# Optimization experiments

Measured on AMD Instinct MI355X. Metric: run time of the kernel, lower is better.

## Reference

```python
import jax, jax.numpy as jnp
import numpy as np

# Synthetic layered DAG: 8 node-layers of width N -> 7 masked dense layers.
B = 4096        # batch
N = 2048        # nodes per DAG layer (= in_features = out_features)
DEPTH = 7       # number of weight layers (len(L) - 1)
DENSITY = 0.25  # fraction of predecessor edges present (mask sparsity)


def setup_inputs() -> dict:
    key = jax.random.key(0)
    kx, kw, km = jax.random.split(key, 3)
    x = jax.random.normal(kx, (B, N), dtype=jnp.float32)
    # Mask M: [DEPTH, N+1, N]; random 0/1 edges, last row (bias) all ones.
    m = (jax.random.uniform(km, (DEPTH, N + 1, N)) < DENSITY).astype(jnp.float32)
    M = m.at[:, -1, :].set(1.0)
    # Kaiming-uniform per column: bound = 1/sqrt(nnz_j) (torch code's init),
    # nonzero only at masked positions (W initialized to zeros elsewhere).
    nnz = jnp.maximum(M.sum(axis=1, keepdims=True), 1.0)  # [DEPTH,1,N]
    u = jax.random.uniform(kw, (DEPTH, N + 1, N), minval=-1.0, maxval=1.0)
    W = (u / jnp.sqrt(nnz)) * M
    return {"x": x, "W": W, "M": M}


def reference(x, W, M):
    # activations buffer semantics collapse to a per-layer chain because each
    # layer's preds are exactly the previous DAG layer; sinks = last layer.
    def step(acts, wm):
        w, m = wm  # [N+1, N] each
        h = jnp.concatenate(
            [acts, jnp.ones((acts.shape[0], 1), acts.dtype)], axis=1)  # [B, N+1]
        acts = jax.nn.relu(h @ (m * w))  # masked dense matmul + ReLU
        return acts, None

    out, _ = jax.lax.scan(step, x, (W, M))
    return out  # [B, N] activations of sink nodes
```

## Files before the change

kernel.cpp:

```cpp
#include <hip/hip_runtime.h>
#include <hip/hip_bf16.h>

typedef __bf16 bf16_t;
typedef __bf16 v8bf __attribute__((ext_vector_type(8)));
typedef __bf16 v4bf __attribute__((ext_vector_type(4)));
typedef float  v4f  __attribute__((ext_vector_type(4)));

#define B_ROWS 4096
#define N_COLS 2048
#define K_FULL 2049
#define KK     2048
#define DEPTH  7

#define BM 128
#define BN 128
#define BK 128
#define NKT (KK / BK)

__global__ __launch_bounds__(256) void wt_kernel(const float* __restrict__ W,
                                                 bf16_t* __restrict__ Wt,
                                                 float* __restrict__ Bias) {
  __shared__ float t[64][129];
  const int l  = blockIdx.z;
  const int k0 = blockIdx.x * 128;
  const int n0 = blockIdx.y * 64;
  const int tid = threadIdx.x;
  const int r   = tid >> 4;
  const int c4  = (tid & 15) * 4;
  const float* Wl = W + (size_t)l * K_FULL * N_COLS;
#pragma unroll
  for (int it = 0; it < 8; ++it) {
    const int kk = r + it * 16;
    const float4 v = *(const float4*)&Wl[(size_t)(k0 + kk) * N_COLS + n0 + c4];
    t[c4 + 0][kk] = v.x;
    t[c4 + 1][kk] = v.y;
    t[c4 + 2][kk] = v.z;
    t[c4 + 3][kk] = v.w;
  }
  if (k0 == 0 && tid < 16) {
    *(float4*)&Bias[(size_t)l * N_COLS + n0 + tid * 4] =
        *(const float4*)&Wl[(size_t)KK * N_COLS + n0 + tid * 4];
  }
  __syncthreads();
  bf16_t* Wtl = Wt + (size_t)l * N_COLS * KK;
  const int g = tid & 15;
#pragma unroll
  for (int it = 0; it < 4; ++it) {
    const int n = r + it * 16;
    v8bf o;
#pragma unroll
    for (int j = 0; j < 8; ++j) o[j] = (bf16_t)t[n][g * 8 + j];
    *(v8bf*)&Wtl[(size_t)(n0 + n) * KK + k0 + g * 8] = o;
  }
}

__global__ __launch_bounds__(256) void init_kernel(const float* __restrict__ x,
                                                   bf16_t* __restrict__ A0) {
  const int c4 = (blockIdx.x * 256 + threadIdx.x) * 4;
  const int r  = blockIdx.y;
  const float4 v = *(const float4*)&x[(size_t)r * N_COLS + c4];
  v4bf o;
  o[0] = (bf16_t)v.x; o[1] = (bf16_t)v.y; o[2] = (bf16_t)v.z; o[3] = (bf16_t)v.w;
  *(v4bf*)&A0[(size_t)r * N_COLS + c4] = o;
}

__global__ __launch_bounds__(512, 4) void gemm_kernel(
    const bf16_t* __restrict__ A, const bf16_t* __restrict__ Bt,
    const float* __restrict__ bias,
    bf16_t* __restrict__ Cn, float* __restrict__ Co) {
  __shared__ __align__(16) char smem[65536];
  bf16_t* As = (bf16_t*)smem;
  bf16_t* Bs = (bf16_t*)(smem + 32768);

  const int bid = blockIdx.x;
  const int swz = (bid & 7) * 64 + (bid >> 3);
  const int bx  = swz & 15;
  const int by  = swz >> 4;

  const int tid  = threadIdx.x;
  const int wave = tid >> 6;
  const int lane = tid & 63;
  const int q    = wave & 3;
  const int kgrp = wave >> 2;
  const int m0 = by * BM;
  const int n0 = bx * BN;
  const int wm = (q & 1) * 64;
  const int wn = (q >> 1) * 64;
  const int quad = lane >> 4;
  const int l16  = lane & 15;

  int aoff[4], boff[4];
#pragma unroll
  for (int c = 0; c < 4; ++c) {
    const int gran = wave * 256 + c * 64 + lane;
    const int srow = gran >> 4;
    const int scol = ((gran & 15) ^ (srow & 15)) << 3;
    aoff[c] = (m0 + srow) * KK + scol;
    boff[c] = (n0 + srow) * KK + scol;
  }

  v4f acc[4][4] = {};

  for (int kt = 0; kt < NKT; ++kt) {
    const int kbase = kt * BK;
    __syncthreads();
#pragma unroll
    for (int c = 0; c < 4; ++c) {
      __builtin_amdgcn_global_load_lds(
          (const __attribute__((address_space(1))) void*)(A + aoff[c] + kbase),
          (__attribute__((address_space(3))) void*)((char*)As + wave * 4096 + c * 1024),
          16, 0, 0);
    }
#pragma unroll
    for (int c = 0; c < 4; ++c) {
      __builtin_amdgcn_global_load_lds(
          (const __attribute__((address_space(1))) void*)(Bt + boff[c] + kbase),
          (__attribute__((address_space(3))) void*)((char*)Bs + wave * 4096 + c * 1024),
          16, 0, 0);
    }
    __syncthreads();

#pragma unroll
    for (int ks = 0; ks < 2; ++ks) {
      v8bf af[4], bfr[4];
      const int kg = kgrp * 8 + ks * 4 + quad;
#pragma unroll
      for (int i = 0; i < 4; ++i) {
        const int arow = wm + i * 16 + l16;
        af[i] = *(const v8bf*)&As[arow * BK + ((kg ^ (arow & 15)) << 3)];
      }
#pragma unroll
      for (int j = 0; j < 4; ++j) {
        const int brow = wn + j * 16 + l16;
        bfr[j] = *(const v8bf*)&Bs[brow * BK + ((kg ^ (brow & 15)) << 3)];
      }
#pragma unroll
      for (int i = 0; i < 4; ++i)
#pragma unroll
        for (int j = 0; j < 4; ++j)
          acc[i][j] = __builtin_amdgcn_mfma_f32_16x16x32_bf16(af[i], bfr[j],
                                                              acc[i][j], 0, 0, 0);
    }
  }

  __syncthreads();
  float* red = (float*)smem;
#pragma unroll
  for (int j = 0; j < 4; ++j) {
    if (kgrp == 0) {
      *(v4f*)(red + q * 4096 + 2 * 1024 + j * 256 + lane * 4) = acc[2][j];
      *(v4f*)(red + q * 4096 + 3 * 1024 + j * 256 + lane * 4) = acc[3][j];
    } else {
      *(v4f*)(red + q * 4096 + 0 * 1024 + j * 256 + lane * 4) = acc[0][j];
      *(v4f*)(red + q * 4096 + 1 * 1024 + j * 256 + lane * 4) = acc[1][j];
    }
  }
  __syncthreads();
#pragma unroll
  for (int j = 0; j < 4; ++j) {
    if (kgrp == 0) {
      acc[0][j] += *(const v4f*)(red + q * 4096 + 0 * 1024 + j * 256 + lane * 4);
      acc[1][j] += *(const v4f*)(red + q * 4096 + 1 * 1024 + j * 256 + lane * 4);
    } else {
      acc[2][j] += *(const v4f*)(red + q * 4096 + 2 * 1024 + j * 256 + lane * 4);
      acc[3][j] += *(const v4f*)(red + q * 4096 + 3 * 1024 + j * 256 + lane * 4);
    }
  }

  float bv[4];
#pragma unroll
  for (int j = 0; j < 4; ++j) bv[j] = bias[n0 + wn + j * 16 + l16];
  const int i0 = kgrp * 2;
#pragma unroll
  for (int ii = 0; ii < 2; ++ii) {
#pragma unroll
    for (int j = 0; j < 4; ++j) {
      v4f a = (kgrp == 0) ? acc[ii][j] : acc[2 + ii][j];
#pragma unroll
      for (int r = 0; r < 4; ++r) {
        float v = a[r] + bv[j];
        v = v > 0.0f ? v : 0.0f;
        const int row = m0 + wm + (i0 + ii) * 16 + quad * 4 + r;
        const int col = n0 + wn + j * 16 + l16;
        if (Co) Co[(size_t)row * N_COLS + col] = v;
        else    Cn[(size_t)row * N_COLS + col] = (bf16_t)v;
      }
    }
  }
}

extern "C" void kernel_launch(void* const* d_in, const int* in_sizes, int n_in,
                              void* d_out, int out_size, void* d_ws, size_t ws_size,
                              hipStream_t stream) {
  const float* x = (const float*)d_in[0];
  const float* W = (const float*)d_in[1];
  float* out = (float*)d_out;

  char* ws = (char*)d_ws;
  const size_t wtBytes = (size_t)DEPTH * N_COLS * KK * sizeof(bf16_t);
  const size_t aBytes  = (size_t)B_ROWS * N_COLS * sizeof(bf16_t);
  bf16_t* Wt   = (bf16_t*)ws;
  bf16_t* A0   = (bf16_t*)(ws + wtBytes);
  bf16_t* A1   = (bf16_t*)(ws + wtBytes + aBytes);
  float*  Bias = (float*)(ws + wtBytes + 2 * aBytes);

  wt_kernel<<<dim3(KK / 128, N_COLS / 64, DEPTH), 256, 0, stream>>>(W, Wt, Bias);
  init_kernel<<<dim3(N_COLS / 4 / 256, B_ROWS), 256, 0, stream>>>(x, A0);

  bf16_t* bufs[2] = {A0, A1};
  for (int l = 0; l < DEPTH; ++l) {
    const bf16_t* Ain = bufs[l & 1];
    bf16_t* Aout      = bufs[(l + 1) & 1];
    const bf16_t* Bl  = Wt + (size_t)l * N_COLS * KK;
    const float* bl   = Bias + (size_t)l * N_COLS;
    const bool last   = (l == DEPTH - 1);
    gemm_kernel<<<dim3((B_ROWS / BM) * (N_COLS / BN)), 512, 0, stream>>>(
        Ain, Bl, bl, last ? nullptr : Aout, last ? out : nullptr);
  }
}
```

Baseline: 475.8 us.

## Double-buffer LDS tiles with BK=64 to overlap global loads with MFMA

Halves the K tile to 64 and splits the 64KB LDS into two buffers, so the next tile's global_load_lds is issued before computing on the current one, with one barrier per iteration. The aim is to hide global-memory latency behind MFMA work instead of stalling on a load-then-sync each step. LDS addressing and the XOR swizzle are rewritten for 8 granules per row. The cost is twice as many loop iterations and barriers. Each wave now reads only one K-slice per tile, and the loads may not be complete when the buffer is read, since there is no explicit vmcnt wait.

```diff
diff --git a/kernel.cpp b/kernel.cpp
--- a/kernel.cpp
+++ b/kernel.cpp
@@ -14,7 +14,7 @@
 
 #define BM 128
 #define BN 128
-#define BK 128
+#define BK 64
 #define NKT (KK / BK)
 
 __global__ __launch_bounds__(256) void wt_kernel(const float* __restrict__ W,
@@ -69,8 +69,6 @@
     const float* __restrict__ bias,
     bf16_t* __restrict__ Cn, float* __restrict__ Co) {
   __shared__ __align__(16) char smem[65536];
-  bf16_t* As = (bf16_t*)smem;
-  bf16_t* Bs = (bf16_t*)(smem + 32768);
 
   const int bid = blockIdx.x;
   const int swz = (bid & 7) * 64 + (bid >> 3);
@@ -89,61 +87,68 @@
   const int quad = lane >> 4;
   const int l16  = lane & 15;
 
-  int aoff[4], boff[4];
-#pragma unroll
-  for (int c = 0; c < 4; ++c) {
-    const int gran = wave * 256 + c * 64 + lane;
-    const int srow = gran >> 4;
-    const int scol = ((gran & 15) ^ (srow & 15)) << 3;
-    aoff[c] = (m0 + srow) * KK + scol;
-    boff[c] = (n0 + srow) * KK + scol;
-  }
+  int aoff[2], boff[2];
+#pragma unroll
+  for (int c = 0; c < 2; ++c) {
+    const int gg  = c * 512 + tid;
+    const int row = gg >> 3;
+    const int sc  = ((gg & 7) ^ (row & 7)) << 3;
+    aoff[c] = (m0 + row) * KK + sc;
+    boff[c] = (n0 + row) * KK + sc;
+  }
+
+  const int X = ((kgrp * 4 + quad) ^ (l16 & 7)) << 4;
+  int ra[4], rb[4];
+#pragma unroll
+  for (int i = 0; i < 4; ++i) ra[i] = (wm + i * 16 + l16) * 128 + X;
+#pragma unroll
+  for (int j = 0; j < 4; ++j) rb[j] = (wn + j * 16 + l16) * 128 + X;
+
+  auto stage = [&](int b, int kb) {
+    char* dA = smem + b * 32768;
+    char* dB = dA + 16384;
+#pragma unroll
+    for (int c = 0; c < 2; ++c) {
+      __builtin_amdgcn_global_load_lds(
+          (const __attribute__((address_space(1))) void*)(A + aoff[c] + kb),
+          (__attribute__((address_space(3))) void*)(dA + c * 8192 + tid * 16),
+          16, 0, 0);
+    }
+#pragma unroll
+    for (int c = 0; c < 2; ++c) {
+      __builtin_amdgcn_global_load_lds(
+          (const __attribute__((address_space(1))) void*)(Bt + boff[c] + kb),
+          (__attribute__((address_space(3))) void*)(dB + c * 8192 + tid * 16),
+          16, 0, 0);
+    }
+  };
 
   v4f acc[4][4] = {};
 
+  stage(0, 0);
+  __syncthreads();
+
+#pragma unroll 2
   for (int kt = 0; kt < NKT; ++kt) {
-    const int kbase = kt * BK;
+    const int cur = kt & 1;
+    if (kt + 1 < NKT) stage(cur ^ 1, (kt + 1) * BK);
+
+    const char* ab = smem + cur * 32768;
+    const char* bb = ab + 16384;
+    v8bf af[4], bfr[4];
+#pragma unroll
+    for (int i = 0; i < 4; ++i) af[i]  = *(const v8bf*)(ab + ra[i]);
+#pragma unroll
+    for (int j = 0; j < 4; ++j) bfr[j] = *(const v8bf*)(bb + rb[j]);
+#pragma unroll
+    for (int i = 0; i < 4; ++i)
+#pragma unroll
+      for (int j = 0; j < 4; ++j)
+        acc[i][j] = __builtin_amdgcn_mfma_f32_16x16x32_bf16(af[i], bfr[j],
+                                                            acc[i][j], 0, 0, 0);
     __syncthreads();
-#pragma unroll
-    for (int c = 0; c < 4; ++c) {
-      __builtin_amdgcn_global_load_lds(
-          (const __attribute__((address_space(1))) void*)(A + aoff[c] + kbase),
-          (__attribute__((address_space(3))) void*)((char*)As + wave * 4096 + c * 1024),
-          16, 0, 0);
-    }
-#pragma unroll
-    for (int c = 0; c < 4; ++c) {
-      __builtin_amdgcn_global_load_lds(
-          (const __attribute__((address_space(1))) void*)(Bt + boff[c] + kbase),
-          (__attribute__((address_space(3))) void*)((char*)Bs + wave * 4096 + c * 1024),
-          16, 0, 0);
-    }
-    __syncthreads();
-
-#pragma unroll
-    for (int ks = 0; ks < 2; ++ks) {
-      v8bf af[4], bfr[4];
-      const int kg = kgrp * 8 + ks * 4 + quad;
-#pragma unroll
-      for (int i = 0; i < 4; ++i) {
-        const int arow = wm + i * 16 + l16;
-        af[i] = *(const v8bf*)&As[arow * BK + ((kg ^ (arow & 15)) << 3)];
-      }
-#pragma unroll
-      for (int j = 0; j < 4; ++j) {
-        const int brow = wn + j * 16 + l16;
-        bfr[j] = *(const v8bf*)&Bs[brow * BK + ((kg ^ (brow & 15)) << 3)];
-      }
-#pragma unroll
-      for (int i = 0; i < 4; ++i)
-#pragma unroll
-        for (int j = 0; j < 4; ++j)
-          acc[i][j] = __builtin_amdgcn_mfma_f32_16x16x32_bf16(af[i], bfr[j],
-                                                              acc[i][j], 0, 0, 0);
-    }
-  }
-
-  __syncthreads();
+  }
+
   float* red = (float*)smem;
 #pragma unroll
   for (int j = 0; j < 4; ++j) {
```

Result: no change. 469.8 us (-1.3%).
